# Optimization experiments

Hardware: AMD Instinct MI355X
Metric: run time of the kernel (lower is better)

The kernel has to match this reference:

```python
import jax, jax.numpy as jnp
import numpy as np

N_NODES = 100000
N_EDGES = 1600000
N_GRAPHS = 256
F_IN = 54


def setup_inputs() -> dict:
    key = jax.random.key(0)
    ks = jax.random.split(key, 16)
    x = jax.random.normal(ks[0], (N_NODES, F_IN), dtype=jnp.float32)
    edge_index = jax.random.randint(ks[1], (2, N_EDGES), 0, N_NODES, dtype=jnp.int32)
    batch = jnp.sort(jax.random.randint(ks[2], (N_NODES,), 0, N_GRAPHS, dtype=jnp.int32))

    def lin(k, fi, fo):
        kw, kb = jax.random.split(k)
        lim = 1.0 / np.sqrt(fi)
        W = jax.random.uniform(kw, (fi, fo), minval=-lim, maxval=lim, dtype=jnp.float32)
        b = jax.random.uniform(kb, (fo,), minval=-lim, maxval=lim, dtype=jnp.float32)
        return W, b

    W1, b1 = lin(ks[3], 54, 54)
    W2, b2 = lin(ks[4], 54, 108)
    W3, b3 = lin(ks[5], 108, 216)
    Wf1, bf1 = lin(ks[6], 216, 1024)
    Wf2, bf2 = lin(ks[7], 1024, 128)
    return {"x": x, "edge_index": edge_index, "batch": batch,
            "W1": W1, "b1": b1, "W2": W2, "b2": b2, "W3": W3, "b3": b3,
            "Wf1": Wf1, "bf1": bf1, "Wf2": Wf2, "bf2": bf2}


def _gcn_norm(edge_index, n):
    # add self-loops, symmetric degree normalization (PyG GCNConv default)
    loop = jnp.arange(n, dtype=edge_index.dtype)
    row = jnp.concatenate([edge_index[0], loop])
    col = jnp.concatenate([edge_index[1], loop])
    deg = jax.ops.segment_sum(jnp.ones_like(col, dtype=jnp.float32), col, num_segments=n)
    dinv = jnp.where(deg > 0, jax.lax.rsqrt(deg), 0.0)
    norm = dinv[row] * dinv[col]
    return row, col, norm


def _gcn_conv(x, row, col, norm, W, b, n):
    h = x @ W                                  # [N, Fout]
    msg = h[row] * norm[:, None]               # [E+N, Fout] gather + scale
    out = jax.ops.segment_sum(msg, col, num_segments=n)  # scatter-add
    return out + b


def reference(x, edge_index, batch, W1, b1, W2, b2, W3, b3, Wf1, bf1, Wf2, bf2):
    n = x.shape[0]
    row, col, norm = _gcn_norm(edge_index, n)
    h = jax.nn.relu(_gcn_conv(x, row, col, norm, W1, b1, n))
    h = jax.nn.relu(_gcn_conv(h, row, col, norm, W2, b2, n))
    h = jax.nn.relu(_gcn_conv(h, row, col, norm, W3, b3, n))
    # global mean pool per graph
    sums = jax.ops.segment_sum(h, batch, num_segments=N_GRAPHS)
    cnts = jax.ops.segment_sum(jnp.ones((n,), jnp.float32), batch, num_segments=N_GRAPHS)
    pooled = sums / jnp.maximum(cnts, 1.0)[:, None]   # [G, 216]
    g = jax.nn.relu(pooled @ Wf1 + bf1)               # dropout = identity (eval)
    return g @ Wf2 + bf2                              # [G, 128]
```

## Files before the change

kernel.cpp:

```cpp
#include <hip/hip_runtime.h>


typedef _Float16 f16;
typedef _Float16 f16x2 __attribute__((ext_vector_type(2)));
typedef _Float16 f16x8 __attribute__((ext_vector_type(8)));
typedef float f32x4 __attribute__((ext_vector_type(4)));

static __host__ __device__ inline int cdiv(int a, int b) { return (a + b - 1) / b; }

constexpr int BSPAN = 512;
constexpr int EPB   = 4096;
constexpr int EPT   = EPB / 256;

template <int V>
__device__ __forceinline__ void vload(float* d, const float* s) {
    if constexpr (V == 1) { d[0] = s[0]; }
    else if constexpr (V == 2) { float2 t = *reinterpret_cast<const float2*>(s); d[0] = t.x; d[1] = t.y; }
    else { float4 t = *reinterpret_cast<const float4*>(s); d[0] = t.x; d[1] = t.y; d[2] = t.z; d[3] = t.w; }
}

__device__ __forceinline__ void wpack_one(const float* W, f16* Wb, int K, int F,
                                          int KT, int idx) {
    int j = idx & 7;
    int lane = (idx >> 3) & 63;
    int fi = idx >> 9;
    int kt = fi % KT;
    int nt = fi / KT;
    int k = kt * 32 + (lane >> 4) * 8 + j;
    int nn = nt * 16 + (lane & 15);
    Wb[idx] = (k < K && nn < F) ? (f16)W[k * F + nn] : (f16)0.f;
}
__global__ void k_wpack3(const float* __restrict__ W1, const float* __restrict__ W2,
                         const float* __restrict__ W3, f16* __restrict__ w1b,
                         f16* __restrict__ w2b, f16* __restrict__ w3b) {
    constexpr int T1 = 4 * 2 * 512;
    constexpr int T2 = 7 * 2 * 512;
    constexpr int T3 = 14 * 4 * 512;
    int idx = blockIdx.x * blockDim.x + threadIdx.x;
    if (idx < T1) wpack_one(W1, w1b, 54, 54, 2, idx);
    else if (idx < T1 + T2) wpack_one(W2, w2b, 54, 108, 2, idx - T1);
    else if (idx < T1 + T2 + T3) wpack_one(W3, w3b, 108, 216, 4, idx - T1 - T2);
}

__global__ void k_setup(float* psum, int nf, int* bktCnt, int* bktCur) {
    int i = blockIdx.x * blockDim.x + threadIdx.x;
    if (i < nf) psum[i] = 0.f;
    if (i < 256) { bktCnt[i] = 0; bktCur[i] = 0; }
}

__global__ __launch_bounds__(256) void k_bkt_hist(const int* __restrict__ col,
                                                  int* bktCnt, int e, int nb) {
    __shared__ int hist[256];
    int t = threadIdx.x;
    hist[t] = 0;
    __syncthreads();
    int base = blockIdx.x * EPB;
#pragma unroll
    for (int j = 0; j < EPT; j++) {
        int idx = base + j * 256 + t;
        if (idx < e) atomicAdd(&hist[col[idx] >> 9], 1);
    }
    __syncthreads();
    if (t < nb && hist[t] > 0) atomicAdd(&bktCnt[t], hist[t]);
}

__device__ __forceinline__ int scan256_ex(int* sbuf, int v, int t) {
    sbuf[t] = v;
    __syncthreads();
    for (int off = 1; off < 256; off <<= 1) {
        int x = sbuf[t];
        int y = (t >= off) ? sbuf[t - off] : 0;
        __syncthreads();
        sbuf[t] = x + y;
        __syncthreads();
    }
    return sbuf[t] - v;
}

__global__ __launch_bounds__(256) void k_bkt_part(const int* __restrict__ row,
                                                  const int* __restrict__ col,
                                                  const int* __restrict__ bktCnt,
                                                  int* bktCur, unsigned int* __restrict__ ebuf,
                                                  int e, int nb) {
    __shared__ int sbuf[256];
    __shared__ int hist[256];
    __shared__ int base[256];
    __shared__ int lcur[256];
    int t = threadIdx.x;
    int boff = scan256_ex(sbuf, (t < nb) ? bktCnt[t] : 0, t);
    hist[t] = 0; lcur[t] = 0;
    __syncthreads();
    int bs = blockIdx.x * EPB;
    unsigned int pk[EPT];
    int b[EPT];
#pragma unroll
    for (int j = 0; j < EPT; j++) {
        int idx = bs + j * 256 + t;
        if (idx < e) {
            int c = col[idx];
            pk[j] = ((unsigned int)(c & (BSPAN - 1)) << 17) | (unsigned int)row[idx];
            b[j] = c >> 9;
            atomicAdd(&hist[b[j]], 1);
        } else b[j] = -1;
    }
    __syncthreads();
    if (t < nb && hist[t] > 0) base[t] = boff + atomicAdd(&bktCur[t], hist[t]);
    __syncthreads();
#pragma unroll
    for (int j = 0; j < EPT; j++) {
        if (b[j] >= 0) {
            int lofs = atomicAdd(&lcur[b[j]], 1);
            ebuf[base[b[j]] + lofs] = pk[j];
        }
    }
}

__global__ __launch_bounds__(256) void k_bkt_build(const unsigned int* __restrict__ ebuf,
                                                   const int* __restrict__ bktCnt,
                                                   int* __restrict__ rowptr,
                                                   float* __restrict__ dinv,
                                                   int* __restrict__ eSrc,
                                                   int n, int nb) {
    __shared__ int sbuf[256];
    __shared__ int hist[BSPAN];
    __shared__ int cur[BSPAN];
    int t = threadIdx.x;
    int bkt = blockIdx.x;

    int boff_ex = scan256_ex(sbuf, (t < nb) ? bktCnt[t] : 0, t);
    __shared__ int boff_s, cnt_s;
    if (t == bkt) boff_s = boff_ex;
    if (t == 0) cnt_s = bktCnt[bkt];
    hist[t] = 0; hist[t + 256] = 0;
    __syncthreads();
    int es = boff_s, ee = boff_s + cnt_s;

    for (int i = es + t; i < ee; i += 256)
        atomicAdd(&hist[ebuf[i] >> 17], 1);
    __syncthreads();

    int h0 = hist[2 * t], h1 = hist[2 * t + 1];
    __syncthreads();
    int ex = scan256_ex(sbuf, h0 + h1, t);
    int e0 = es + ex, e1 = e0 + h0;

    int node0 = bkt * BSPAN;
    int n0 = node0 + 2 * t, n1 = node0 + 2 * t + 1;
    if (n0 <= n) rowptr[n0] = e0;
    if (n1 <= n) rowptr[n1] = e1;
    if (n0 < n) dinv[n0] = rsqrtf((float)(h0 + 1));
    if (n1 < n) dinv[n1] = rsqrtf((float)(h1 + 1));
    cur[2 * t] = e0; cur[2 * t + 1] = e1;
    __syncthreads();

    for (int i = es + t; i < ee; i += 256) {
        unsigned int p = ebuf[i];
        int slot = atomicAdd(&cur[p >> 17], 1);
        eSrc[slot] = (int)(p & 0x1FFFFu);
    }
}

template <int F, int RS>
__global__ void k_prescale(const float* __restrict__ x, const float* __restrict__ dinv,
                           f16* __restrict__ xs, int n) {
    constexpr int CH = F / 2;
    int idx = blockIdx.x * blockDim.x + threadIdx.x;
    if (idx >= n * CH) return;
    int node = idx / CH;
    int c = idx - node * CH;
    float d = dinv[node];
    float v[2];
    vload<2>(v, x + (long long)node * F + c * 2);
    f16x2 h;
    h[0] = (f16)(v[0] * d);
    h[1] = (f16)(v[1] * d);
    *reinterpret_cast<f16x2*>(xs + (long long)node * RS + c * 2) = h;
}

__global__ void k_find_start(const int* __restrict__ batch, int* start, int n, int g) {
    int i = blockIdx.x * blockDim.x + threadIdx.x;
    if (i >= n) return;
    int b = batch[i];
    int bp = (i == 0) ? -1 : batch[i - 1];
    for (int gg = bp + 1; gg <= b; gg++) start[gg] = i;
    if (i == n - 1)
        for (int gg = b + 1; gg <= g; gg++) start[gg] = n;
}

template <int F, int RS>
__global__ __launch_bounds__(256) void k_gatherw(
        const int* __restrict__ rowptr, const int* __restrict__ eSrc,
        const float* __restrict__ dinv, const f16* __restrict__ hs,
        f16* __restrict__ out, int n) {
    constexpr int CGN = RS / 8;
    constexpr int EPW = 64 / CGN;
    int wave = threadIdx.x >> 6;
    int lane = threadIdx.x & 63;
    int eslot = lane / CGN;
    int cg = lane & (CGN - 1);
    int node = blockIdx.x * 4 + wave;
    if (node >= n) return;
    int ch0 = cg * 8;
    int lim = F - ch0;
    if (lim > 8) lim = 8;
    if (lim < 0) lim = 0;

    int rs_ = rowptr[node], re = rowptr[node + 1];
    int deg = re - rs_;
    int myidx = 0;
    if (lane < deg) myidx = eSrc[rs_ + lane];

    const f16x8* src = reinterpret_cast<const f16x8*>(hs);
    float acc[8];
#pragma unroll
    for (int j = 0; j < 8; j++) acc[j] = 0.f;

    if (eslot == 0) {
        f16x8 v = src[(long long)node * CGN + cg];
#pragma unroll
        for (int j = 0; j < 8; j++) acc[j] += (float)v[j];
    }

    int nfull = deg < 64 ? deg : 64;
    int base = 0;
    for (; base + 4 * EPW <= nfull; base += 4 * EPW) {
        int s0 = __shfl(myidx, base + eslot);
        int s1 = __shfl(myidx, base + EPW + eslot);
        int s2 = __shfl(myidx, base + 2 * EPW + eslot);
        int s3 = __shfl(myidx, base + 3 * EPW + eslot);
        f16x8 v0 = src[(long long)s0 * CGN + cg];
        f16x8 v1 = src[(long long)s1 * CGN + cg];
        f16x8 v2 = src[(long long)s2 * CGN + cg];
        f16x8 v3 = src[(long long)s3 * CGN + cg];
#pragma unroll
        for (int j = 0; j < 8; j++)
            acc[j] += ((float)v0[j] + (float)v1[j]) + ((float)v2[j] + (float)v3[j]);
    }
    for (; base + 2 * EPW <= nfull; base += 2 * EPW) {
        int s0 = __shfl(myidx, base + eslot);
        int s1 = __shfl(myidx, base + EPW + eslot);
        f16x8 v0 = src[(long long)s0 * CGN + cg];
        f16x8 v1 = src[(long long)s1 * CGN + cg];
#pragma unroll
        for (int j = 0; j < 8; j++) acc[j] += (float)v0[j] + (float)v1[j];
    }
    for (; base + EPW <= nfull; base += EPW) {
        int s = __shfl(myidx, base + eslot);
        f16x8 v = src[(long long)s * CGN + cg];
#pragma unroll
        for (int j = 0; j < 8; j++) acc[j] += (float)v[j];
    }
    if (base < nfull) {
        int idx = base + eslot;
        int s = __shfl(myidx, idx < 63 ? idx : 63);
        if (idx < nfull) {
            f16x8 v = src[(long long)s * CGN + cg];
#pragma unroll
            for (int j = 0; j < 8; j++) acc[j] += (float)v[j];
        }
    }
    for (int e = rs_ + 64 + eslot; e < re; e += EPW) {
        int s = eSrc[e];
        f16x8 v = src[(long long)s * CGN + cg];
#pragma unroll
        for (int j = 0; j < 8; j++) acc[j] += (float)v[j];
    }

#pragma unroll
    for (int j = 0; j < 8; j++)
        if (j >= lim) acc[j] = 0.f;
#pragma unroll
    for (int m = CGN; m < 64; m <<= 1)
#pragma unroll
        for (int j = 0; j < 8; j++) acc[j] += __shfl_xor(acc[j], m);

    if (eslot == 0) {
        float di = dinv[node];
        f16x8 o;
#pragma unroll
        for (int j = 0; j < 8; j++) o[j] = (f16)(acc[j] * di);
        *reinterpret_cast<f16x8*>(out + (long long)node * RS + ch0) = o;
    }
}

template <int KTILES, int NTILES, int K, int FOUT, int OSTR, bool POOL>
__global__ __launch_bounds__(256) void k_gemm_mfma(
        const f16* __restrict__ in, const f16* __restrict__ Wb,
        const float* __restrict__ bias, const float* __restrict__ dinv,
        const int* __restrict__ batch, f16* __restrict__ outh,
        float* __restrict__ psum, int n) {
    constexpr int KPAD = KTILES * 32;
    constexpr int KP   = KPAD + 8;
    constexpr int V8   = KPAD / 8;
    constexpr int NSLOT = 4;

    __shared__ f16 a_lds[64 * KP];
    __shared__ float psum_l[POOL ? NSLOT * FOUT : 1];

    int t = threadIdx.x;
    int node0 = blockIdx.x * 64;

    const f16x8* inp = reinterpret_cast<const f16x8*>(in);
    for (int f = t; f < 64 * V8; f += 256) {
        int node = f / V8;
        int v = f - node * V8;
        f16x8 val = {};
        if (node0 + node < n) val = inp[(long long)(node0 + node) * V8 + v];
        *reinterpret_cast<f16x8*>(&a_lds[node * KP + v * 8]) = val;
    }
    if (POOL) {
        for (int i = t; i < NSLOT * FOUT; i += 256) psum_l[i] = 0.f;
    }
    __syncthreads();

    int w = t >> 6;
    int lane = t & 63;
    int quad = lane >> 4;
    int col = lane & 15;

    f16x8 afr[KTILES];
#pragma unroll
    for (int kt = 0; kt < KTILES; kt++)
        afr[kt] = *reinterpret_cast<const f16x8*>(
            &a_lds[(16 * w + col) * KP + kt * 32 + quad * 8]);

    int nodeC = node0 + 16 * w + quad * 4;
    float dv[4];
    int gb[4];
#pragma unroll
    for (int r = 0; r < 4; r++) {
        int nd = nodeC + r;
        bool valid = nd < n;
        if (POOL) {
            gb[r] = valid ? batch[nd] : -1;
            dv[r] = 0.f;
        } else {
            dv[r] = valid ? dinv[nd] : 0.f;
            gb[r] = -1;
        }
    }
    int g0 = POOL ? batch[node0] : 0;

    const f16x8* wb = reinterpret_cast<const f16x8*>(Wb);
#pragma unroll
    for (int nt = 0; nt < NTILES; nt++) {
        f16x8 bfr[KTILES];
#pragma unroll
        for (int kt = 0; kt < KTILES; kt++)
            bfr[kt] = wb[(nt * KTILES + kt) * 64 + lane];
        f32x4 acc = {0.f, 0.f, 0.f, 0.f};
#pragma unroll
        for (int kt = 0; kt < KTILES; kt++)
            acc = __builtin_amdgcn_mfma_f32_16x16x32_f16(afr[kt], bfr[kt], acc, 0, 0, 0);

        int ch = nt * 16 + col;
        if (ch < FOUT) {
            float bval = bias[ch];
            if (POOL) {
                if (gb[0] == gb[3] && gb[0] >= 0) {
                    float s = fmaxf(acc[0] + bval, 0.f) + fmaxf(acc[1] + bval, 0.f)
                            + fmaxf(acc[2] + bval, 0.f) + fmaxf(acc[3] + bval, 0.f);
                    int slot = gb[0] - g0;
                    if (slot < NSLOT) atomicAdd(&psum_l[slot * FOUT + ch], s);
                    else atomicAdd(&psum[gb[0] * FOUT + ch], s);
                } else {
#pragma unroll
                    for (int r = 0; r < 4; r++) {
                        if (gb[r] < 0) continue;
                        float v = fmaxf(acc[r] + bval, 0.f);
                        int slot = gb[r] - g0;
                        if (slot < NSLOT) atomicAdd(&psum_l[slot * FOUT + ch], v);
                        else atomicAdd(&psum[gb[r] * FOUT + ch], v);
                    }
                }
            } else {
#pragma unroll
                for (int r = 0; r < 4; r++) {
                    int nd = nodeC + r;
                    if (nd < n)
                        outh[(long long)nd * OSTR + ch] =
                            (f16)(fmaxf(acc[r] + bval, 0.f) * dv[r]);
                }
            }
        }
    }

    if (POOL) {
        __syncthreads();
        int lastNode = node0 + 63;
        if (lastNode >= n) lastNode = n - 1;
        int nsl = batch[lastNode] - g0 + 1;
        if (nsl > NSLOT) nsl = NSLOT;
        for (int f = t; f < nsl * FOUT; f += 256) {
            float v = psum_l[f];
            if (v != 0.f) atomicAdd(&psum[(g0 + f / FOUT) * FOUT + (f % FOUT)], v);
        }
    }
}

__global__ void k_fc1(const float* __restrict__ P, const int* __restrict__ start,
                      const float* __restrict__ W, const float* __restrict__ bias,
                      float* __restrict__ out) {
    int row = blockIdx.x >> 2;
    int o = (blockIdx.x & 3) * 256 + threadIdx.x;
    int cnt = start[row + 1] - start[row];
    float scale = 1.0f / fmaxf((float)cnt, 1.0f);
    __shared__ float prow[216];
    if (threadIdx.x < 216) prow[threadIdx.x] = P[row * 216 + threadIdx.x] * scale;
    __syncthreads();
    float acc = bias[o];
    for (int k = 0; k < 216; k++) acc += prow[k] * W[k * 1024 + o];
    out[row * 1024 + o] = fmaxf(acc, 0.f);
}
__global__ void k_fc2(const float* __restrict__ G, const float* __restrict__ W,
                      const float* __restrict__ bias, float* __restrict__ out) {
    int row = blockIdx.x;
    int o = threadIdx.x;
    __shared__ float grow[1024];
    for (int k = threadIdx.x; k < 1024; k += 128) grow[k] = G[row * 1024 + k];
    __syncthreads();
    float acc = bias[o];
    for (int k = 0; k < 1024; k++) acc += grow[k] * W[k * 128 + o];
    out[row * 128 + o] = acc;
}

extern "C" void kernel_launch(void* const* d_in, const int* in_sizes, int n_in,
                              void* d_out, int out_size, void* d_ws, size_t ws_size,
                              hipStream_t stream) {
    const float* x     = (const float*)d_in[0];
    const int*   ei    = (const int*)d_in[1];
    const int*   batch = (const int*)d_in[2];
    const float* W1  = (const float*)d_in[3];
    const float* b1  = (const float*)d_in[4];
    const float* W2  = (const float*)d_in[5];
    const float* b2  = (const float*)d_in[6];
    const float* W3  = (const float*)d_in[7];
    const float* b3  = (const float*)d_in[8];
    const float* Wf1 = (const float*)d_in[9];
    const float* bf1 = (const float*)d_in[10];
    const float* Wf2 = (const float*)d_in[11];
    const float* bf2 = (const float*)d_in[12];
    float* out = (float*)d_out;

    const int N = in_sizes[0] / 54;
    const int E = in_sizes[1] / 2;
    const int G = 256;
    const int* row = ei;
    const int* col = ei + E;
    const int NB = cdiv(N, BSPAN);
    const int NBLK_A = cdiv(E, EPB);

    char* ws = (char*)d_ws;
    size_t off = 0;
    auto carve = [&](size_t bytes) {
        void* p = ws + off;
        off += (bytes + 255) & ~(size_t)255;
        return p;
    };
    int*   rowptr  = (int*)carve((size_t)(N + 1) * 4);
    int*   bktCnt  = (int*)carve(256 * 4);
    int*   bktCur  = (int*)carve(256 * 4);
    int*   eSrc    = (int*)carve((size_t)E * 4);
    float* dinv    = (float*)carve((size_t)N * 4);
    f16*   xs      = (f16*)carve((size_t)N * 64 * 2);
    f16*   hsbuf   = (f16*)carve((size_t)N * 128 * 2);
    f16*   bufA    = (f16*)carve((size_t)N * 128 * 2);
    unsigned int* ebuf = (unsigned int*)carve((size_t)E * 4);
    float* psum    = (float*)carve((size_t)G * 216 * 4);
    float* gbuf    = (float*)carve((size_t)G * 1024 * 4);
    int*   start   = (int*)carve((size_t)(G + 1) * 4);
    f16*   w1b     = (f16*)carve((size_t)4 * 2 * 512 * 2);
    f16*   w2b     = (f16*)carve((size_t)7 * 2 * 512 * 2);
    f16*   w3b     = (f16*)carve((size_t)14 * 4 * 512 * 2);

    const int T = 256;

    k_setup<<<cdiv(G * 216, T), T, 0, stream>>>(psum, G * 216, bktCnt, bktCur);
    k_wpack3<<<cdiv((4 * 2 + 7 * 2 + 14 * 4) * 512, T), T, 0, stream>>>(
        W1, W2, W3, w1b, w2b, w3b);
    k_find_start<<<cdiv(N, T), T, 0, stream>>>(batch, start, N, G);

    k_bkt_hist<<<NBLK_A, 256, 0, stream>>>(col, bktCnt, E, NB);
    k_bkt_part<<<NBLK_A, 256, 0, stream>>>(row, col, bktCnt, bktCur, ebuf, E, NB);
    k_bkt_build<<<NB, 256, 0, stream>>>(ebuf, bktCnt, rowptr, dinv, eSrc, N, NB);

    k_prescale<54, 64><<<cdiv(N * 27, T), T, 0, stream>>>(x, dinv, xs, N);

    const int GB = cdiv(N, 64);

    k_gatherw<54, 64><<<cdiv(N, 4), 256, 0, stream>>>(rowptr, eSrc, dinv, xs, bufA, N);
    k_gemm_mfma<2, 4, 54, 54, 64, false><<<GB, 256, 0, stream>>>(
        bufA, w1b, b1, dinv, nullptr, hsbuf, nullptr, N);

    k_gatherw<54, 64><<<cdiv(N, 4), 256, 0, stream>>>(rowptr, eSrc, dinv, hsbuf, bufA, N);
    k_gemm_mfma<2, 7, 54, 108, 128, false><<<GB, 256, 0, stream>>>(
        bufA, w2b, b2, dinv, nullptr, hsbuf, nullptr, N);

    k_gatherw<108, 128><<<cdiv(N, 4), 256, 0, stream>>>(rowptr, eSrc, dinv, hsbuf, bufA, N);
    k_gemm_mfma<4, 14, 108, 216, 0, true><<<GB, 256, 0, stream>>>(
        bufA, w3b, b3, nullptr, batch, nullptr, psum, N);

    k_fc1<<<G * 4, T, 0, stream>>>(psum, start, Wf1, bf1, gbuf);
    k_fc2<<<G, 128, 0, stream>>>(gbuf, Wf2, bf2, out);
}
```

Before: 400.1 us.

## Fuse neighbor gather into MFMA GEMM per GCN layer, unroll bucket build loops

Merges the per-node gather-aggregate kernel with the following MFMA GEMM, so each block aggregates its 64 nodes straight into LDS and then multiplies, dropping the intermediate global buffer write and read and one launch per layer. Ping-pong buffers are rearranged because the gather source and the output must now differ. The histogram and scatter loops in the bucket build are also unrolled by four to expose more memory-level parallelism. The cost is fewer blocks (N/64 instead of N/4), with each wave serially processing 16 nodes, which can reduce latency hiding for the irregular gathers.

```diff
diff --git a/kernel.cpp b/kernel.cpp
--- a/kernel.cpp
+++ b/kernel.cpp
@@ -135,8 +135,17 @@
     __syncthreads();
     int es = boff_s, ee = boff_s + cnt_s;
 
-    for (int i = es + t; i < ee; i += 256)
-        atomicAdd(&hist[ebuf[i] >> 17], 1);
+    {
+        int i = es + t;
+        for (; i + 3 * 256 < ee; i += 4 * 256) {
+            unsigned p0 = ebuf[i], p1 = ebuf[i + 256], p2 = ebuf[i + 512], p3 = ebuf[i + 768];
+            atomicAdd(&hist[p0 >> 17], 1);
+            atomicAdd(&hist[p1 >> 17], 1);
+            atomicAdd(&hist[p2 >> 17], 1);
+            atomicAdd(&hist[p3 >> 17], 1);
+        }
+        for (; i < ee; i += 256) atomicAdd(&hist[ebuf[i] >> 17], 1);
+    }
     __syncthreads();
 
     int h0 = hist[2 * t], h1 = hist[2 * t + 1];
@@ -153,10 +162,24 @@
     cur[2 * t] = e0; cur[2 * t + 1] = e1;
     __syncthreads();
 
-    for (int i = es + t; i < ee; i += 256) {
-        unsigned int p = ebuf[i];
-        int slot = atomicAdd(&cur[p >> 17], 1);
-        eSrc[slot] = (int)(p & 0x1FFFFu);
+    {
+        int i = es + t;
+        for (; i + 3 * 256 < ee; i += 4 * 256) {
+            unsigned p0 = ebuf[i], p1 = ebuf[i + 256], p2 = ebuf[i + 512], p3 = ebuf[i + 768];
+            int s0 = atomicAdd(&cur[p0 >> 17], 1);
+            int s1 = atomicAdd(&cur[p1 >> 17], 1);
+            int s2 = atomicAdd(&cur[p2 >> 17], 1);
+            int s3 = atomicAdd(&cur[p3 >> 17], 1);
+            eSrc[s0] = (int)(p0 & 0x1FFFFu);
+            eSrc[s1] = (int)(p1 & 0x1FFFFu);
+            eSrc[s2] = (int)(p2 & 0x1FFFFu);
+            eSrc[s3] = (int)(p3 & 0x1FFFFu);
+        }
+        for (; i < ee; i += 256) {
+            unsigned int p = ebuf[i];
+            int slot = atomicAdd(&cur[p >> 17], 1);
+            eSrc[slot] = (int)(p & 0x1FFFFu);
+        }
     }
 }
 
@@ -187,134 +210,123 @@
         for (int gg = b + 1; gg <= g; gg++) start[gg] = n;
 }
 
-template <int F, int RS>
-__global__ __launch_bounds__(256) void k_gatherw(
+template <int F, int KTILES, int NTILES, int FOUT, int OSTR, bool POOL>
+__global__ __launch_bounds__(256) void k_gcn_fused(
         const int* __restrict__ rowptr, const int* __restrict__ eSrc,
         const float* __restrict__ dinv, const f16* __restrict__ hs,
-        f16* __restrict__ out, int n) {
-    constexpr int CGN = RS / 8;
-    constexpr int EPW = 64 / CGN;
-    int wave = threadIdx.x >> 6;
-    int lane = threadIdx.x & 63;
+        const f16* __restrict__ Wb, const float* __restrict__ bias,
+        const int* __restrict__ batch, f16* __restrict__ outh,
+        float* __restrict__ psum, int n) {
+    constexpr int KPAD = KTILES * 32;
+    constexpr int KP   = KPAD + 8;
+    constexpr int CGN  = KPAD / 8;
+    constexpr int EPW  = 64 / CGN;
+    constexpr int NSLOT = 4;
+
+    __shared__ __align__(16) f16 a_lds[64 * KP];
+    __shared__ float psum_l[POOL ? NSLOT * FOUT : 1];
+
+    int t = threadIdx.x;
+    int node0 = blockIdx.x * 64;
+    int w = t >> 6;
+    int lane = t & 63;
     int eslot = lane / CGN;
     int cg = lane & (CGN - 1);
-    int node = blockIdx.x * 4 + wave;
-    if (node >= n) return;
     int ch0 = cg * 8;
     int lim = F - ch0;
     if (lim > 8) lim = 8;
     if (lim < 0) lim = 0;
 
-    int rs_ = rowptr[node], re = rowptr[node + 1];
-    int deg = re - rs_;
-    int myidx = 0;
-    if (lane < deg) myidx = eSrc[rs_ + lane];
-
-    const f16x8* src = reinterpret_cast<const f16x8*>(hs);
-    float acc[8];
-#pragma unroll
-    for (int j = 0; j < 8; j++) acc[j] = 0.f;
-
-    if (eslot == 0) {
-        f16x8 v = src[(long long)node * CGN + cg];
-#pragma unroll
-        for (int j = 0; j < 8; j++) acc[j] += (float)v[j];
-    }
-
-    int nfull = deg < 64 ? deg : 64;
-    int base = 0;
-    for (; base + 4 * EPW <= nfull; base += 4 * EPW) {
-        int s0 = __shfl(myidx, base + eslot);
-        int s1 = __shfl(myidx, base + EPW + eslot);
-        int s2 = __shfl(myidx, base + 2 * EPW + eslot);
-        int s3 = __shfl(myidx, base + 3 * EPW + eslot);
-        f16x8 v0 = src[(long long)s0 * CGN + cg];
-        f16x8 v1 = src[(long long)s1 * CGN + cg];
-        f16x8 v2 = src[(long long)s2 * CGN + cg];
-        f16x8 v3 = src[(long long)s3 * CGN + cg];
-#pragma unroll
-        for (int j = 0; j < 8; j++)
-            acc[j] += ((float)v0[j] + (float)v1[j]) + ((float)v2[j] + (float)v3[j]);
-    }
-    for (; base + 2 * EPW <= nfull; base += 2 * EPW) {
-        int s0 = __shfl(myidx, base + eslot);
-        int s1 = __shfl(myidx, base + EPW + eslot);
-        f16x8 v0 = src[(long long)s0 * CGN + cg];
-        f16x8 v1 = src[(long long)s1 * CGN + cg];
-#pragma unroll
-        for (int j = 0; j < 8; j++) acc[j] += (float)v0[j] + (float)v1[j];
-    }
-    for (; base + EPW <= nfull; base += EPW) {
-        int s = __shfl(myidx, base + eslot);
-        f16x8 v = src[(long long)s * CGN + cg];
-#pragma unroll
-        for (int j = 0; j < 8; j++) acc[j] += (float)v[j];
-    }
-    if (base < nfull) {
-        int idx = base + eslot;
-        int s = __shfl(myidx, idx < 63 ? idx : 63);
-        if (idx < nfull) {
-            f16x8 v = src[(long long)s * CGN + cg];
-#pragma unroll
-            for (int j = 0; j < 8; j++) acc[j] += (float)v[j];
-        }
-    }
-    for (int e = rs_ + 64 + eslot; e < re; e += EPW) {
-        int s = eSrc[e];
-        f16x8 v = src[(long long)s * CGN + cg];
-#pragma unroll
-        for (int j = 0; j < 8; j++) acc[j] += (float)v[j];
-    }
-
-#pragma unroll
-    for (int j = 0; j < 8; j++)
-        if (j >= lim) acc[j] = 0.f;
-#pragma unroll
-    for (int m = CGN; m < 64; m <<= 1)
-#pragma unroll
-        for (int j = 0; j < 8; j++) acc[j] += __shfl_xor(acc[j], m);
-
-    if (eslot == 0) {
-        float di = dinv[node];
-        f16x8 o;
-#pragma unroll
-        for (int j = 0; j < 8; j++) o[j] = (f16)(acc[j] * di);
-        *reinterpret_cast<f16x8*>(out + (long long)node * RS + ch0) = o;
-    }
-}
-
-template <int KTILES, int NTILES, int K, int FOUT, int OSTR, bool POOL>
-__global__ __launch_bounds__(256) void k_gemm_mfma(
-        const f16* __restrict__ in, const f16* __restrict__ Wb,
-        const float* __restrict__ bias, const float* __restrict__ dinv,
-        const int* __restrict__ batch, f16* __restrict__ outh,
-        float* __restrict__ psum, int n) {
-    constexpr int KPAD = KTILES * 32;
-    constexpr int KP   = KPAD + 8;
-    constexpr int V8   = KPAD / 8;
-    constexpr int NSLOT = 4;
-
-    __shared__ f16 a_lds[64 * KP];
-    __shared__ float psum_l[POOL ? NSLOT * FOUT : 1];
-
-    int t = threadIdx.x;
-    int node0 = blockIdx.x * 64;
-
-    const f16x8* inp = reinterpret_cast<const f16x8*>(in);
-    for (int f = t; f < 64 * V8; f += 256) {
-        int node = f / V8;
-        int v = f - node * V8;
-        f16x8 val = {};
-        if (node0 + node < n) val = inp[(long long)(node0 + node) * V8 + v];
-        *reinterpret_cast<f16x8*>(&a_lds[node * KP + v * 8]) = val;
-    }
     if (POOL) {
         for (int i = t; i < NSLOT * FOUT; i += 256) psum_l[i] = 0.f;
     }
-    __syncthreads();
-
-    int w = t >> 6;
-    int lane = t & 63;
+
+    const f16x8* src = reinterpret_cast<const f16x8*>(hs);
+
+    for (int i = 0; i < 16; i++) {
+        int node = node0 + w * 16 + i;
+        float acc[8];
+#pragma unroll
+        for (int j = 0; j < 8; j++) acc[j] = 0.f;
+        float di = 0.f;
+
+        if (node < n) {
+            int rs_ = rowptr[node], re = rowptr[node + 1];
+            int deg = re - rs_;
+            int myidx = 0;
+            if (lane < deg) myidx = eSrc[rs_ + lane];
+
+            if (eslot == 0) {
+                f16x8 v = src[(long long)node * CGN + cg];
+#pragma unroll
+                for (int j = 0; j < 8; j++) acc[j] += (float)v[j];
+            }
+
+            int nfull = deg < 64 ? deg : 64;
+            int base = 0;
+            for (; base + 4 * EPW <= nfull; base += 4 * EPW) {
+                int s0 = __shfl(myidx, base + eslot);
+                int s1 = __shfl(myidx, base + EPW + eslot);
+                int s2 = __shfl(myidx, base + 2 * EPW + eslot);
+                int s3 = __shfl(myidx, base + 3 * EPW + eslot);
+                f16x8 v0 = src[(long long)s0 * CGN + cg];
+                f16x8 v1 = src[(long long)s1 * CGN + cg];
+                f16x8 v2 = src[(long long)s2 * CGN + cg];
+                f16x8 v3 = src[(long long)s3 * CGN + cg];
+#pragma unroll
+                for (int j = 0; j < 8; j++)
+                    acc[j] += ((float)v0[j] + (float)v1[j]) + ((float)v2[j] + (float)v3[j]);
+            }
+            for (; base + 2 * EPW <= nfull; base += 2 * EPW) {
+                int s0 = __shfl(myidx, base + eslot);
+                int s1 = __shfl(myidx, base + EPW + eslot);
+                f16x8 v0 = src[(long long)s0 * CGN + cg];
+                f16x8 v1 = src[(long long)s1 * CGN + cg];
+#pragma unroll
+                for (int j = 0; j < 8; j++) acc[j] += (float)v0[j] + (float)v1[j];
+            }
+            for (; base + EPW <= nfull; base += EPW) {
+                int s = __shfl(myidx, base + eslot);
+                f16x8 v = src[(long long)s * CGN + cg];
+#pragma unroll
+                for (int j = 0; j < 8; j++) acc[j] += (float)v[j];
+            }
+            if (base < nfull) {
+                int idx = base + eslot;
+                int s = __shfl(myidx, idx < 63 ? idx : 63);
+                if (idx < nfull) {
+                    f16x8 v = src[(long long)s * CGN + cg];
+#pragma unroll
+                    for (int j = 0; j < 8; j++) acc[j] += (float)v[j];
+                }
+            }
+            for (int e = rs_ + 64 + eslot; e < re; e += EPW) {
+                int s = eSrc[e];
+                f16x8 v = src[(long long)s * CGN + cg];
+#pragma unroll
+                for (int j = 0; j < 8; j++) acc[j] += (float)v[j];
+            }
+
+#pragma unroll
+            for (int j = 0; j < 8; j++)
+                if (j >= lim) acc[j] = 0.f;
+#pragma unroll
+            for (int m = CGN; m < 64; m <<= 1)
+#pragma unroll
+                for (int j = 0; j < 8; j++) acc[j] += __shfl_xor(acc[j], m);
+
+            di = dinv[node];
+        }
+
+        if (eslot == 0) {
+            f16x8 o;
+#pragma unroll
+            for (int j = 0; j < 8; j++) o[j] = (f16)(acc[j] * di);
+            *reinterpret_cast<f16x8*>(&a_lds[(w * 16 + i) * KP + ch0]) = o;
+        }
+    }
+    __syncthreads();
+
     int quad = lane >> 4;
     int col = lane & 15;
 
@@ -488,17 +500,14 @@
 
     const int GB = cdiv(N, 64);
 
-    k_gatherw<54, 64><<<cdiv(N, 4), 256, 0, stream>>>(rowptr, eSrc, dinv, xs, bufA, N);
-    k_gemm_mfma<2, 4, 54, 54, 64, false><<<GB, 256, 0, stream>>>(
-        bufA, w1b, b1, dinv, nullptr, hsbuf, nullptr, N);
-
-    k_gatherw<54, 64><<<cdiv(N, 4), 256, 0, stream>>>(rowptr, eSrc, dinv, hsbuf, bufA, N);
-    k_gemm_mfma<2, 7, 54, 108, 128, false><<<GB, 256, 0, stream>>>(
-        bufA, w2b, b2, dinv, nullptr, hsbuf, nullptr, N);
-
-    k_gatherw<108, 128><<<cdiv(N, 4), 256, 0, stream>>>(rowptr, eSrc, dinv, hsbuf, bufA, N);
-    k_gemm_mfma<4, 14, 108, 216, 0, true><<<GB, 256, 0, stream>>>(
-        bufA, w3b, b3, nullptr, batch, nullptr, psum, N);
+    k_gcn_fused<54, 2, 4, 54, 64, false><<<GB, 256, 0, stream>>>(
+        rowptr, eSrc, dinv, xs, w1b, b1, nullptr, hsbuf, nullptr, N);
+
+    k_gcn_fused<54, 2, 7, 108, 128, false><<<GB, 256, 0, stream>>>(
+        rowptr, eSrc, dinv, hsbuf, w2b, b2, nullptr, bufA, nullptr, N);
+
+    k_gcn_fused<108, 4, 14, 216, 0, true><<<GB, 256, 0, stream>>>(
+        rowptr, eSrc, dinv, bufA, w3b, b3, batch, nullptr, psum, N);
 
     k_fc1<<<G * 4, T, 0, stream>>>(psum, start, Wf1, bf1, gbuf);
     k_fc2<<<G, 128, 0, stream>>>(gbuf, Wf2, bf2, out);
```

Measured after the change: 405.2 us. Within noise of the previous version (+1.3%).
